# Performance work log

Hardware: AMD Instinct MI355X
Metric: run time of the kernel (lower is better)

The kernel has to match this reference:

```python
import jax, jax.numpy as jnp
import numpy as np

ALPHA = 0.2          # LeakyReLU negative slope
NEG_INF = -9e15      # mask value from the original code


def setup_inputs() -> dict:
    key = jax.random.key(0)
    k1, k2, k3, k4 = jax.random.split(key, 4)
    B, N, F_in, F_out = 8, 2048, 64, 64
    x = jax.random.normal(k1, (B, N, F_in), dtype=jnp.float32)
    adj = jax.random.randint(k2, (B, N, N), 0, 2, dtype=jnp.int32)
    W = jax.random.normal(k3, (F_in, F_out), dtype=jnp.float32)
    a = jax.random.normal(k4, (2 * F_out, 1), dtype=jnp.float32)
    return {"x": x, "adj": adj, "W": W, "a": a}


def reference(x, adj, W, a):
    # h: [B, N, F_out]
    h = jnp.matmul(x, W)
    F_out = W.shape[1]
    a1 = a[:F_out, 0]   # source half of attention vector
    a2 = a[F_out:, 0]   # target half
    # e_ij = leakyrelu(h_i . a1 + h_j . a2)  -- identical math to the
    # original cat([h_i, h_j]) @ a without materializing [B,N*N,2F].
    s1 = jnp.einsum('bnf,f->bn', h, a1)  # [B, N]
    s2 = jnp.einsum('bnf,f->bn', h, a2)  # [B, N]
    e = jax.nn.leaky_relu(s1[:, :, None] + s2[:, None, :], negative_slope=ALPHA)
    masked = jnp.where(adj > 0, e, NEG_INF)
    attention = jax.nn.softmax(masked, axis=2)  # [B, N, N]
    # dropout p=0.0 / eval mode -> identity
    h_prime = jnp.matmul(attention, h)          # [B, N, F_out]
    return jax.nn.elu(h_prime)                  # concat=True branch
```

## Files before the change

### kernel.cpp

```cpp
#include <hip/hip_runtime.h>
#include <cstdint>

#define LRELU_ALPHA 0.2f
#define NEG_INF -9000000000000000.0f
#define L2E 1.4426950408889634f

typedef __bf16 bf16x8 __attribute__((ext_vector_type(8)));
typedef unsigned short ushortx8 __attribute__((ext_vector_type(8)));
typedef float floatx4 __attribute__((ext_vector_type(4)));
typedef unsigned int uintx4 __attribute__((ext_vector_type(4)));

constexpr int Bb = 8, Nn = 2048, Ff = 64;
constexpr int TJ = 64;
constexpr int SEG = 8;
constexpr int SEGT = (Nn / TJ) / SEG;
constexpr int WIN = SEGT * TJ;
constexpr int WSTR = 264;
constexpr int NROWS = Bb * Nn;

__device__ __forceinline__ unsigned short f2bf(float f) {
    unsigned u = __builtin_bit_cast(unsigned, f);
    u = u + 0x7FFFu + ((u >> 16) & 1u);
    return (unsigned short)(u >> 16);
}

__device__ __forceinline__ unsigned cvt_pk_bf16(float lo, float hi) {
    unsigned r;
    asm("v_cvt_pk_bf16_f32 %0, %1, %2" : "=v"(r) : "v"(lo), "v"(hi));
    return r;
}

__global__ __launch_bounds__(256) void gat_prep(
    const float* __restrict__ x, const float* __restrict__ W, const float* __restrict__ a,
    unsigned short* __restrict__ hT, float* __restrict__ s1g, float* __restrict__ s2g)
{
    constexpr int STR2 = 36;
    __shared__ unsigned short hblk[64 * STR2];
    const int tid = threadIdx.x;
    const int blk = blockIdx.x;
    const int b  = blk >> 6;
    const int i0 = (blk & 63) * 32;
    const int w    = tid >> 6;
    const int lane = tid & 63;

    float wcol[64];
    #pragma unroll
    for (int k = 0; k < 64; ++k) wcol[k] = W[k * 64 + lane];
    const float a1 = a[lane], a2 = a[64 + lane];

    for (int r = 0; r < 8; ++r) {
        const int il = w * 8 + r;
        const int i  = i0 + il;
        const float* xrow = x + ((size_t)(b * Nn + i)) * 64;
        float h0 = 0.f, h1 = 0.f, h2 = 0.f, h3 = 0.f;
        #pragma unroll
        for (int k = 0; k < 64; k += 4) {
            h0 = fmaf(xrow[k],     wcol[k],     h0);
            h1 = fmaf(xrow[k + 1], wcol[k + 1], h1);
            h2 = fmaf(xrow[k + 2], wcol[k + 2], h2);
            h3 = fmaf(xrow[k + 3], wcol[k + 3], h3);
        }
        const float h = (h0 + h1) + (h2 + h3);
        float p1 = h * a1, p2 = h * a2;
        #pragma unroll
        for (int off = 32; off; off >>= 1) {
            p1 += __shfl_xor(p1, off);
            p2 += __shfl_xor(p2, off);
        }
        if (lane == 0) { s1g[b * Nn + i] = p1; s2g[b * Nn + i] = p2; }
        hblk[lane * STR2 + il] = f2bf(h);
    }
    __syncthreads();
    {
        const int f = tid >> 2, c = (tid & 3) * 8;
        uint4 v = *reinterpret_cast<const uint4*>(&hblk[f * STR2 + c]);
        *reinterpret_cast<uint4*>(hT + ((size_t)b * 64 + f) * Nn + i0 + c) = v;
    }
}

__global__ __launch_bounds__(256) void gat_attn(
    const int* __restrict__ adj, const unsigned short* __restrict__ hT,
    const float* __restrict__ s1g, const float* __restrict__ s2g,
    float* __restrict__ m_part, float* __restrict__ l_part, float* __restrict__ O_part)
{
    __shared__ unsigned short hT_lds[64 * WSTR];
    __shared__ float s2_lds[WIN];

    const int tid  = threadIdx.x;
    const int blk  = blockIdx.x;
    const int seg  = blk >> 8;
    const int grp  = blk & 255;
    const int gr0  = grp * 64;
    const int b    = gr0 >> 11;
    const int i0   = gr0 & 2047;
    const int w    = tid >> 6;
    const int lane = tid & 63;
    const int fl   = lane & 15;
    const int q    = lane >> 4;

    const int i = i0 + w * 16 + fl;
    const int j0w = seg * WIN;
    const unsigned short* hTb = hT + (size_t)b * 64 * Nn;

    uint4 stg[8];
    #pragma unroll
    for (int k = 0; k < 8; ++k) {
        const int c = tid + (k << 8);
        stg[k] = *reinterpret_cast<const uint4*>(
            hTb + (size_t)(c >> 5) * Nn + j0w + ((c & 31) << 3));
    }
    const float s2stg = s2g[b * Nn + j0w + tid];
    const float s1v = s1g[b * Nn + i];
    const int* adj_row = adj + ((size_t)(b * Nn + i)) * Nn;

    int4 adjv[4];
    {
        const int* arow = adj_row + j0w;
        const int4* ap0 = reinterpret_cast<const int4*>(arow + q * 8);
        adjv[0] = ap0[0]; adjv[1] = ap0[1];
        const int4* ap1 = reinterpret_cast<const int4*>(arow + 32 + q * 8);
        adjv[2] = ap1[0]; adjv[3] = ap1[1];
    }

    #pragma unroll
    for (int k = 0; k < 8; ++k) {
        const int c = tid + (k << 8);
        *reinterpret_cast<uint4*>(&hT_lds[(c >> 5) * WSTR + ((c & 31) << 3)]) = stg[k];
    }
    s2_lds[tid] = s2stg;
    __syncthreads();

    float m = NEG_INF, l = 0.f;
    floatx4 C[4] = {};

    for (int jt = 0; jt < SEGT; ++jt) {
        const int jloc = jt * TJ;

        int4 nadj[4] = {};
        if (jt + 1 < SEGT) {
            const int* nrow = adj_row + j0w + jloc + TJ;
            const int4* ap0 = reinterpret_cast<const int4*>(nrow + q * 8);
            nadj[0] = ap0[0]; nadj[1] = ap0[1];
            const int4* ap1 = reinterpret_cast<const int4*>(nrow + 32 + q * 8);
            nadj[2] = ap1[0]; nadj[3] = ap1[1];
        }

        float p[16];
        const int* av = reinterpret_cast<const int*>(adjv);
        #pragma unroll
        for (int t = 0; t < 2; ++t) {
            float s2v[8];
            *reinterpret_cast<float4*>(&s2v[0]) =
                *reinterpret_cast<const float4*>(&s2_lds[jloc + t * 32 + q * 8]);
            *reinterpret_cast<float4*>(&s2v[4]) =
                *reinterpret_cast<const float4*>(&s2_lds[jloc + t * 32 + q * 8 + 4]);
            #pragma unroll
            for (int jj = 0; jj < 8; ++jj) {
                float ev = s1v + s2v[jj];
                ev = fmaxf(ev, LRELU_ALPHA * ev);
                p[t * 8 + jj] = (av[t * 8 + jj] > 0) ? ev : NEG_INF;
            }
        }
        float tmax = p[0];
        #pragma unroll
        for (int k = 1; k < 16; ++k) tmax = fmaxf(tmax, p[k]);
        tmax = fmaxf(tmax, __shfl_xor(tmax, 16));
        tmax = fmaxf(tmax, __shfl_xor(tmax, 32));
        const float m_new = fmaxf(m, tmax);
        const float alpha_s = exp2f((m - m_new) * L2E);
        m = m_new;

        float tsum = 0.f;
        #pragma unroll
        for (int k = 0; k < 16; ++k) {
            p[k] = exp2f((p[k] - m_new) * L2E);
            tsum += p[k];
        }
        tsum += __shfl_xor(tsum, 16);
        tsum += __shfl_xor(tsum, 32);
        l = l * alpha_s + tsum;

        uintx4 pa, pb;
        #pragma unroll
        for (int d = 0; d < 4; ++d) {
            pa[d] = cvt_pk_bf16(p[2 * d],     p[2 * d + 1]);
            pb[d] = cvt_pk_bf16(p[8 + 2 * d], p[8 + 2 * d + 1]);
        }
        const bf16x8 A0 = __builtin_bit_cast(bf16x8, pa);
        const bf16x8 A1 = __builtin_bit_cast(bf16x8, pb);

        float ac[4];
        #pragma unroll
        for (int r = 0; r < 4; ++r) ac[r] = __shfl(alpha_s, q * 4 + r);
        #pragma unroll
        for (int u = 0; u < 4; ++u)
            #pragma unroll
            for (int r = 0; r < 4; ++r) C[u][r] *= ac[r];

        __builtin_amdgcn_s_setprio(1);
        #pragma unroll
        for (int u = 0; u < 4; ++u) {
            const bf16x8 B0 = *reinterpret_cast<const bf16x8*>(
                &hT_lds[(u * 16 + fl) * WSTR + jloc + q * 8]);
            C[u] = __builtin_amdgcn_mfma_f32_16x16x32_bf16(A0, B0, C[u], 0, 0, 0);
            const bf16x8 B1 = *reinterpret_cast<const bf16x8*>(
                &hT_lds[(u * 16 + fl) * WSTR + jloc + 32 + q * 8]);
            C[u] = __builtin_amdgcn_mfma_f32_16x16x32_bf16(A1, B1, C[u], 0, 0, 0);
        }
        __builtin_amdgcn_s_setprio(0);

        adjv[0] = nadj[0]; adjv[1] = nadj[1]; adjv[2] = nadj[2]; adjv[3] = nadj[3];
    }

    if (q == 0) {
        const int ri = b * Nn + i;
        m_part[seg * NROWS + ri] = m;
        l_part[seg * NROWS + ri] = l;
    }
    #pragma unroll
    for (int u = 0; u < 4; ++u) {
        #pragma unroll
        for (int r = 0; r < 4; ++r) {
            const int orow = i0 + w * 16 + q * 4 + r;
            O_part[((size_t)seg * NROWS + b * Nn + orow) * 64 + u * 16 + fl] = C[u][r];
        }
    }
}

__global__ __launch_bounds__(256) void gat_merge(
    const float* __restrict__ m_part, const float* __restrict__ l_part,
    const float* __restrict__ O_part, float* __restrict__ out)
{
    const int tid = threadIdx.x;
    const int ri  = blockIdx.x * 4 + (tid >> 6);
    const int f   = tid & 63;

    float mv[SEG];
    #pragma unroll
    for (int s = 0; s < SEG; ++s) mv[s] = m_part[s * NROWS + ri];
    float mstar = mv[0];
    #pragma unroll
    for (int s = 1; s < SEG; ++s) mstar = fmaxf(mstar, mv[s]);

    float lsum = 0.f, acc = 0.f;
    #pragma unroll
    for (int s = 0; s < SEG; ++s) {
        const float wgt = exp2f((mv[s] - mstar) * L2E);
        lsum += l_part[s * NROWS + ri] * wgt;
        acc  += O_part[((size_t)s * NROWS + ri) * 64 + f] * wgt;
    }
    float v = acc / lsum;
    v = (v > 0.f) ? v : (exp2f(v * L2E) - 1.f);
    out[(size_t)ri * 64 + f] = v;
}

extern "C" void kernel_launch(void* const* d_in, const int* in_sizes, int n_in,
                              void* d_out, int out_size, void* d_ws, size_t ws_size,
                              hipStream_t stream) {
    const float* x   = (const float*)d_in[0];
    const int*   adj = (const int*)d_in[1];
    const float* W   = (const float*)d_in[2];
    const float* a   = (const float*)d_in[3];
    float* out = (float*)d_out;

    char* p = (char*)d_ws;
    unsigned short* hT = (unsigned short*)p;  p += (size_t)Bb * 64 * Nn * sizeof(unsigned short);
    float* s1 = (float*)p;                    p += (size_t)NROWS * sizeof(float);
    float* s2 = (float*)p;                    p += (size_t)NROWS * sizeof(float);
    float* m_part = (float*)p;                p += (size_t)SEG * NROWS * sizeof(float);
    float* l_part = (float*)p;                p += (size_t)SEG * NROWS * sizeof(float);
    float* O_part = (float*)p;

    gat_prep<<<dim3(Bb * Nn / 32), dim3(256), 0, stream>>>(x, W, a, hT, s1, s2);
    gat_attn<<<dim3(SEG * (NROWS / 64)), dim3(256), 0, stream>>>(
        adj, hT, s1, s2, m_part, l_part, O_part);
    gat_merge<<<dim3(NROWS / 4), dim3(256), 0, stream>>>(m_part, l_part, O_part, out);
}
```

Measured before the change: 237.0 us.

## Cut j-split to two segments with double-staged hT windows and lazy rescale

Each block now covers 1024 columns in 2 segments instead of 8. It streams 256-column windows of hT and s2 through registers into LDS, prefetching the next window while computing the current one. This reduces the partial-result write and merge traffic and the grid size. The online-softmax rescale of the accumulators is skipped when no row max increases in the wave. In exchange there are fewer blocks (a 512 grid, down from 2048) and extra barriers per window.

```diff
diff --git a/kernel.cpp b/kernel.cpp
--- a/kernel.cpp
+++ b/kernel.cpp
@@ -6,15 +6,16 @@
 #define L2E 1.4426950408889634f
 
 typedef __bf16 bf16x8 __attribute__((ext_vector_type(8)));
-typedef unsigned short ushortx8 __attribute__((ext_vector_type(8)));
 typedef float floatx4 __attribute__((ext_vector_type(4)));
 typedef unsigned int uintx4 __attribute__((ext_vector_type(4)));
 
 constexpr int Bb = 8, Nn = 2048, Ff = 64;
 constexpr int TJ = 64;
-constexpr int SEG = 8;
-constexpr int SEGT = (Nn / TJ) / SEG;
-constexpr int WIN = SEGT * TJ;
+constexpr int SEG = 2;
+constexpr int SEGJ = Nn / SEG;
+constexpr int WIN = 256;
+constexpr int NW = SEGJ / WIN;
+constexpr int NTILE = SEGJ / TJ;
 constexpr int WSTR = 264;
 constexpr int NROWS = Bb * Nn;
 
@@ -99,117 +100,134 @@
     const int q    = lane >> 4;
 
     const int i = i0 + w * 16 + fl;
-    const int j0w = seg * WIN;
+    const int jseg0 = seg * SEGJ;
     const unsigned short* hTb = hT + (size_t)b * 64 * Nn;
+    const int* adj_row = adj + ((size_t)(b * Nn + i)) * Nn + jseg0;
+    const float* s2b = s2g + b * Nn + jseg0;
+    const float s1v = s1g[b * Nn + i];
 
     uint4 stg[8];
-    #pragma unroll
-    for (int k = 0; k < 8; ++k) {
-        const int c = tid + (k << 8);
-        stg[k] = *reinterpret_cast<const uint4*>(
-            hTb + (size_t)(c >> 5) * Nn + j0w + ((c & 31) << 3));
-    }
-    const float s2stg = s2g[b * Nn + j0w + tid];
-    const float s1v = s1g[b * Nn + i];
-    const int* adj_row = adj + ((size_t)(b * Nn + i)) * Nn;
-
-    int4 adjv[4];
-    {
-        const int* arow = adj_row + j0w;
+    float s2stg;
+
+    auto stage_issue = [&](int wn) {
+        const int jb = wn * WIN;
+        #pragma unroll
+        for (int k = 0; k < 8; ++k) {
+            const int c = tid + (k << 8);
+            stg[k] = *reinterpret_cast<const uint4*>(
+                hTb + (size_t)(c >> 5) * Nn + jseg0 + jb + ((c & 31) << 3));
+        }
+        s2stg = s2b[jb + tid];
+    };
+    auto stage_write = [&]() {
+        #pragma unroll
+        for (int k = 0; k < 8; ++k) {
+            const int c = tid + (k << 8);
+            *reinterpret_cast<uint4*>(&hT_lds[(c >> 5) * WSTR + ((c & 31) << 3)]) = stg[k];
+        }
+        s2_lds[tid] = s2stg;
+    };
+    auto adj_load = [&](int t, int4 (&av)[4]) {
+        const int* arow = adj_row + t * TJ;
         const int4* ap0 = reinterpret_cast<const int4*>(arow + q * 8);
-        adjv[0] = ap0[0]; adjv[1] = ap0[1];
+        av[0] = ap0[0]; av[1] = ap0[1];
         const int4* ap1 = reinterpret_cast<const int4*>(arow + 32 + q * 8);
-        adjv[2] = ap1[0]; adjv[3] = ap1[1];
-    }
-
-    #pragma unroll
-    for (int k = 0; k < 8; ++k) {
-        const int c = tid + (k << 8);
-        *reinterpret_cast<uint4*>(&hT_lds[(c >> 5) * WSTR + ((c & 31) << 3)]) = stg[k];
-    }
-    s2_lds[tid] = s2stg;
+        av[2] = ap1[0]; av[3] = ap1[1];
+    };
+
+    int4 adjv[4], nadj[4];
+    stage_issue(0);
+    adj_load(0, adjv);
+    stage_write();
     __syncthreads();
 
     float m = NEG_INF, l = 0.f;
     floatx4 C[4] = {};
 
-    for (int jt = 0; jt < SEGT; ++jt) {
-        const int jloc = jt * TJ;
-
-        int4 nadj[4] = {};
-        if (jt + 1 < SEGT) {
-            const int* nrow = adj_row + j0w + jloc + TJ;
-            const int4* ap0 = reinterpret_cast<const int4*>(nrow + q * 8);
-            nadj[0] = ap0[0]; nadj[1] = ap0[1];
-            const int4* ap1 = reinterpret_cast<const int4*>(nrow + 32 + q * 8);
-            nadj[2] = ap1[0]; nadj[3] = ap1[1];
-        }
-
-        float p[16];
-        const int* av = reinterpret_cast<const int*>(adjv);
-        #pragma unroll
-        for (int t = 0; t < 2; ++t) {
-            float s2v[8];
-            *reinterpret_cast<float4*>(&s2v[0]) =
-                *reinterpret_cast<const float4*>(&s2_lds[jloc + t * 32 + q * 8]);
-            *reinterpret_cast<float4*>(&s2v[4]) =
-                *reinterpret_cast<const float4*>(&s2_lds[jloc + t * 32 + q * 8 + 4]);
-            #pragma unroll
-            for (int jj = 0; jj < 8; ++jj) {
-                float ev = s1v + s2v[jj];
-                ev = fmaxf(ev, LRELU_ALPHA * ev);
-                p[t * 8 + jj] = (av[t * 8 + jj] > 0) ? ev : NEG_INF;
-            }
-        }
-        float tmax = p[0];
-        #pragma unroll
-        for (int k = 1; k < 16; ++k) tmax = fmaxf(tmax, p[k]);
-        tmax = fmaxf(tmax, __shfl_xor(tmax, 16));
-        tmax = fmaxf(tmax, __shfl_xor(tmax, 32));
-        const float m_new = fmaxf(m, tmax);
-        const float alpha_s = exp2f((m - m_new) * L2E);
-        m = m_new;
-
-        float tsum = 0.f;
-        #pragma unroll
-        for (int k = 0; k < 16; ++k) {
-            p[k] = exp2f((p[k] - m_new) * L2E);
-            tsum += p[k];
-        }
-        tsum += __shfl_xor(tsum, 16);
-        tsum += __shfl_xor(tsum, 32);
-        l = l * alpha_s + tsum;
-
-        uintx4 pa, pb;
-        #pragma unroll
-        for (int d = 0; d < 4; ++d) {
-            pa[d] = cvt_pk_bf16(p[2 * d],     p[2 * d + 1]);
-            pb[d] = cvt_pk_bf16(p[8 + 2 * d], p[8 + 2 * d + 1]);
-        }
-        const bf16x8 A0 = __builtin_bit_cast(bf16x8, pa);
-        const bf16x8 A1 = __builtin_bit_cast(bf16x8, pb);
-
-        float ac[4];
-        #pragma unroll
-        for (int r = 0; r < 4; ++r) ac[r] = __shfl(alpha_s, q * 4 + r);
-        #pragma unroll
-        for (int u = 0; u < 4; ++u)
-            #pragma unroll
-            for (int r = 0; r < 4; ++r) C[u][r] *= ac[r];
-
-        __builtin_amdgcn_s_setprio(1);
-        #pragma unroll
-        for (int u = 0; u < 4; ++u) {
-            const bf16x8 B0 = *reinterpret_cast<const bf16x8*>(
-                &hT_lds[(u * 16 + fl) * WSTR + jloc + q * 8]);
-            C[u] = __builtin_amdgcn_mfma_f32_16x16x32_bf16(A0, B0, C[u], 0, 0, 0);
-            const bf16x8 B1 = *reinterpret_cast<const bf16x8*>(
-                &hT_lds[(u * 16 + fl) * WSTR + jloc + 32 + q * 8]);
-            C[u] = __builtin_amdgcn_mfma_f32_16x16x32_bf16(A1, B1, C[u], 0, 0, 0);
-        }
-        __builtin_amdgcn_s_setprio(0);
-
-        adjv[0] = nadj[0]; adjv[1] = nadj[1]; adjv[2] = nadj[2]; adjv[3] = nadj[3];
+    for (int wn = 0; wn < NW; ++wn) {
+        if (wn + 1 < NW) stage_issue(wn + 1);
+
+        #pragma unroll
+        for (int jt = 0; jt < WIN / TJ; ++jt) {
+            const int t = wn * (WIN / TJ) + jt;
+            if (t + 1 < NTILE) adj_load(t + 1, nadj);
+            const int jloc = jt * TJ;
+
+            float p[16];
+            const int* av = reinterpret_cast<const int*>(adjv);
+            #pragma unroll
+            for (int tt = 0; tt < 2; ++tt) {
+                float s2v[8];
+                *reinterpret_cast<float4*>(&s2v[0]) =
+                    *reinterpret_cast<const float4*>(&s2_lds[jloc + tt * 32 + q * 8]);
+                *reinterpret_cast<float4*>(&s2v[4]) =
+                    *reinterpret_cast<const float4*>(&s2_lds[jloc + tt * 32 + q * 8 + 4]);
+                #pragma unroll
+                for (int jj = 0; jj < 8; ++jj) {
+                    float ev = s1v + s2v[jj];
+                    ev = fmaxf(ev, LRELU_ALPHA * ev);
+                    p[tt * 8 + jj] = (av[tt * 8 + jj] > 0) ? ev : NEG_INF;
+                }
+            }
+            float tmax = p[0];
+            #pragma unroll
+            for (int k = 1; k < 16; ++k) tmax = fmaxf(tmax, p[k]);
+            tmax = fmaxf(tmax, __shfl_xor(tmax, 16));
+            tmax = fmaxf(tmax, __shfl_xor(tmax, 32));
+            const float m_new = fmaxf(m, tmax);
+
+            if (__any(m_new > m)) {
+                const float alpha_s = exp2f((m - m_new) * L2E);
+                l *= alpha_s;
+                float ac[4];
+                #pragma unroll
+                for (int r = 0; r < 4; ++r) ac[r] = __shfl(alpha_s, q * 4 + r);
+                #pragma unroll
+                for (int u = 0; u < 4; ++u)
+                    #pragma unroll
+                    for (int r = 0; r < 4; ++r) C[u][r] *= ac[r];
+                m = m_new;
+            }
+
+            float tsum = 0.f;
+            #pragma unroll
+            for (int k = 0; k < 16; ++k) {
+                p[k] = exp2f((p[k] - m) * L2E);
+                tsum += p[k];
+            }
+            tsum += __shfl_xor(tsum, 16);
+            tsum += __shfl_xor(tsum, 32);
+            l += tsum;
+
+            uintx4 pa, pb;
+            #pragma unroll
+            for (int d = 0; d < 4; ++d) {
+                pa[d] = cvt_pk_bf16(p[2 * d],     p[2 * d + 1]);
+                pb[d] = cvt_pk_bf16(p[8 + 2 * d], p[8 + 2 * d + 1]);
+            }
+            const bf16x8 A0 = __builtin_bit_cast(bf16x8, pa);
+            const bf16x8 A1 = __builtin_bit_cast(bf16x8, pb);
+
+            __builtin_amdgcn_s_setprio(1);
+            #pragma unroll
+            for (int u = 0; u < 4; ++u) {
+                const bf16x8 B0 = *reinterpret_cast<const bf16x8*>(
+                    &hT_lds[(u * 16 + fl) * WSTR + jloc + q * 8]);
+                C[u] = __builtin_amdgcn_mfma_f32_16x16x32_bf16(A0, B0, C[u], 0, 0, 0);
+                const bf16x8 B1 = *reinterpret_cast<const bf16x8*>(
+                    &hT_lds[(u * 16 + fl) * WSTR + jloc + 32 + q * 8]);
+                C[u] = __builtin_amdgcn_mfma_f32_16x16x32_bf16(A1, B1, C[u], 0, 0, 0);
+            }
+            __builtin_amdgcn_s_setprio(0);
+
+            adjv[0] = nadj[0]; adjv[1] = nadj[1]; adjv[2] = nadj[2]; adjv[3] = nadj[3];
+        }
+
+        if (wn + 1 < NW) {
+            __syncthreads();
+            stage_write();
+            __syncthreads();
+        }
     }
 
     if (q == 0) {
```

Result: slower. 243.0 us (+2.5%).

## Fuse split-K merge into attention kernel with in-block segment reduction

Applied to the files above, without the earlier changes.

Restructures the attention kernel so each 512-thread block handles 16 rows, with 8 waves each covering one 256-column slice. The partial max, sum and output are merged in LDS inside the same block, which removes the separate merge kernel and the global m/l/O partial buffers. The hT and s2 tiles are now read straight from global memory/cache instead of being staged in LDS. Accumulator rescaling is skipped when no lane's running max grows. This trades LDS staging and the next-tile adjacency prefetch for less global traffic and one fewer launch, at the risk of more load latency in the inner loop.

```diff
diff --git a/kernel.cpp b/kernel.cpp
--- a/kernel.cpp
+++ b/kernel.cpp
@@ -6,16 +6,14 @@
 #define L2E 1.4426950408889634f
 
 typedef __bf16 bf16x8 __attribute__((ext_vector_type(8)));
-typedef unsigned short ushortx8 __attribute__((ext_vector_type(8)));
 typedef float floatx4 __attribute__((ext_vector_type(4)));
 typedef unsigned int uintx4 __attribute__((ext_vector_type(4)));
 
 constexpr int Bb = 8, Nn = 2048, Ff = 64;
 constexpr int TJ = 64;
-constexpr int SEG = 8;
-constexpr int SEGT = (Nn / TJ) / SEG;
-constexpr int WIN = SEGT * TJ;
-constexpr int WSTR = 264;
+constexpr int SEGW = 8;
+constexpr int SLICE = Nn / SEGW;
+constexpr int NT = SLICE / TJ;
 constexpr int NROWS = Bb * Nn;
 
 __device__ __forceinline__ unsigned short f2bf(float f) {
@@ -78,87 +76,59 @@
     }
 }
 
-__global__ __launch_bounds__(256) void gat_attn(
+__global__ __launch_bounds__(512, 6) void gat_attn(
     const int* __restrict__ adj, const unsigned short* __restrict__ hT,
     const float* __restrict__ s1g, const float* __restrict__ s2g,
-    float* __restrict__ m_part, float* __restrict__ l_part, float* __restrict__ O_part)
+    float* __restrict__ out)
 {
-    __shared__ unsigned short hT_lds[64 * WSTR];
-    __shared__ float s2_lds[WIN];
+    __shared__ float O_lds[SEGW][16][65];
+    __shared__ float m_lds[SEGW][16];
+    __shared__ float l_lds[SEGW][16];
 
     const int tid  = threadIdx.x;
     const int blk  = blockIdx.x;
-    const int seg  = blk >> 8;
-    const int grp  = blk & 255;
-    const int gr0  = grp * 64;
-    const int b    = gr0 >> 11;
-    const int i0   = gr0 & 2047;
-    const int w    = tid >> 6;
+    const int b    = blk >> 7;
+    const int i0   = (blk & 127) * 16;
+    const int s    = tid >> 6;
     const int lane = tid & 63;
     const int fl   = lane & 15;
     const int q    = lane >> 4;
 
-    const int i = i0 + w * 16 + fl;
-    const int j0w = seg * WIN;
-    const unsigned short* hTb = hT + (size_t)b * 64 * Nn;
-
-    uint4 stg[8];
-    #pragma unroll
-    for (int k = 0; k < 8; ++k) {
-        const int c = tid + (k << 8);
-        stg[k] = *reinterpret_cast<const uint4*>(
-            hTb + (size_t)(c >> 5) * Nn + j0w + ((c & 31) << 3));
-    }
-    const float s2stg = s2g[b * Nn + j0w + tid];
+    const int i = i0 + fl;
     const float s1v = s1g[b * Nn + i];
-    const int* adj_row = adj + ((size_t)(b * Nn + i)) * Nn;
-
-    int4 adjv[4];
-    {
-        const int* arow = adj_row + j0w;
-        const int4* ap0 = reinterpret_cast<const int4*>(arow + q * 8);
-        adjv[0] = ap0[0]; adjv[1] = ap0[1];
-        const int4* ap1 = reinterpret_cast<const int4*>(arow + 32 + q * 8);
-        adjv[2] = ap1[0]; adjv[3] = ap1[1];
-    }
-
-    #pragma unroll
-    for (int k = 0; k < 8; ++k) {
-        const int c = tid + (k << 8);
-        *reinterpret_cast<uint4*>(&hT_lds[(c >> 5) * WSTR + ((c & 31) << 3)]) = stg[k];
-    }
-    s2_lds[tid] = s2stg;
-    __syncthreads();
+    const int* adj_row = adj + ((size_t)(b * Nn + i)) * Nn + s * SLICE;
+    const unsigned short* hTb = hT + (size_t)b * 64 * Nn + s * SLICE;
+    const float* s2b = s2g + b * Nn + s * SLICE;
 
     float m = NEG_INF, l = 0.f;
     floatx4 C[4] = {};
 
-    for (int jt = 0; jt < SEGT; ++jt) {
+    for (int jt = 0; jt < NT; ++jt) {
         const int jloc = jt * TJ;
 
-        int4 nadj[4] = {};
-        if (jt + 1 < SEGT) {
-            const int* nrow = adj_row + j0w + jloc + TJ;
-            const int4* ap0 = reinterpret_cast<const int4*>(nrow + q * 8);
-            nadj[0] = ap0[0]; nadj[1] = ap0[1];
-            const int4* ap1 = reinterpret_cast<const int4*>(nrow + 32 + q * 8);
-            nadj[2] = ap1[0]; nadj[3] = ap1[1];
+        int4 adjv[4];
+        {
+            const int* arow = adj_row + jloc;
+            const int4* ap0 = reinterpret_cast<const int4*>(arow + q * 8);
+            adjv[0] = ap0[0]; adjv[1] = ap0[1];
+            const int4* ap1 = reinterpret_cast<const int4*>(arow + 32 + q * 8);
+            adjv[2] = ap1[0]; adjv[3] = ap1[1];
         }
 
         float p[16];
         const int* av = reinterpret_cast<const int*>(adjv);
         #pragma unroll
-        for (int t = 0; t < 2; ++t) {
+        for (int tt = 0; tt < 2; ++tt) {
             float s2v[8];
             *reinterpret_cast<float4*>(&s2v[0]) =
-                *reinterpret_cast<const float4*>(&s2_lds[jloc + t * 32 + q * 8]);
+                *reinterpret_cast<const float4*>(&s2b[jloc + tt * 32 + q * 8]);
             *reinterpret_cast<float4*>(&s2v[4]) =
-                *reinterpret_cast<const float4*>(&s2_lds[jloc + t * 32 + q * 8 + 4]);
+                *reinterpret_cast<const float4*>(&s2b[jloc + tt * 32 + q * 8 + 4]);
             #pragma unroll
             for (int jj = 0; jj < 8; ++jj) {
                 float ev = s1v + s2v[jj];
                 ev = fmaxf(ev, LRELU_ALPHA * ev);
-                p[t * 8 + jj] = (av[t * 8 + jj] > 0) ? ev : NEG_INF;
+                p[tt * 8 + jj] = (av[tt * 8 + jj] > 0) ? ev : NEG_INF;
             }
         }
         float tmax = p[0];
@@ -167,18 +137,29 @@
         tmax = fmaxf(tmax, __shfl_xor(tmax, 16));
         tmax = fmaxf(tmax, __shfl_xor(tmax, 32));
         const float m_new = fmaxf(m, tmax);
-        const float alpha_s = exp2f((m - m_new) * L2E);
-        m = m_new;
+
+        if (__any(m_new > m)) {
+            const float alpha_s = exp2f((m - m_new) * L2E);
+            l *= alpha_s;
+            float ac[4];
+            #pragma unroll
+            for (int r = 0; r < 4; ++r) ac[r] = __shfl(alpha_s, q * 4 + r);
+            #pragma unroll
+            for (int u = 0; u < 4; ++u)
+                #pragma unroll
+                for (int r = 0; r < 4; ++r) C[u][r] *= ac[r];
+            m = m_new;
+        }
 
         float tsum = 0.f;
         #pragma unroll
         for (int k = 0; k < 16; ++k) {
-            p[k] = exp2f((p[k] - m_new) * L2E);
+            p[k] = exp2f((p[k] - m) * L2E);
             tsum += p[k];
         }
         tsum += __shfl_xor(tsum, 16);
         tsum += __shfl_xor(tsum, 32);
-        l = l * alpha_s + tsum;
+        l += tsum;
 
         uintx4 pa, pb;
         #pragma unroll
@@ -189,69 +170,52 @@
         const bf16x8 A0 = __builtin_bit_cast(bf16x8, pa);
         const bf16x8 A1 = __builtin_bit_cast(bf16x8, pb);
 
-        float ac[4];
-        #pragma unroll
-        for (int r = 0; r < 4; ++r) ac[r] = __shfl(alpha_s, q * 4 + r);
-        #pragma unroll
-        for (int u = 0; u < 4; ++u)
-            #pragma unroll
-            for (int r = 0; r < 4; ++r) C[u][r] *= ac[r];
-
         __builtin_amdgcn_s_setprio(1);
         #pragma unroll
         for (int u = 0; u < 4; ++u) {
             const bf16x8 B0 = *reinterpret_cast<const bf16x8*>(
-                &hT_lds[(u * 16 + fl) * WSTR + jloc + q * 8]);
+                hTb + (size_t)(u * 16 + fl) * Nn + jloc + q * 8);
             C[u] = __builtin_amdgcn_mfma_f32_16x16x32_bf16(A0, B0, C[u], 0, 0, 0);
             const bf16x8 B1 = *reinterpret_cast<const bf16x8*>(
-                &hT_lds[(u * 16 + fl) * WSTR + jloc + 32 + q * 8]);
+                hTb + (size_t)(u * 16 + fl) * Nn + jloc + 32 + q * 8);
             C[u] = __builtin_amdgcn_mfma_f32_16x16x32_bf16(A1, B1, C[u], 0, 0, 0);
         }
         __builtin_amdgcn_s_setprio(0);
-
-        adjv[0] = nadj[0]; adjv[1] = nadj[1]; adjv[2] = nadj[2]; adjv[3] = nadj[3];
-    }
-
-    if (q == 0) {
-        const int ri = b * Nn + i;
-        m_part[seg * NROWS + ri] = m;
-        l_part[seg * NROWS + ri] = l;
-    }
-    #pragma unroll
-    for (int u = 0; u < 4; ++u) {
-        #pragma unroll
-        for (int r = 0; r < 4; ++r) {
-            const int orow = i0 + w * 16 + q * 4 + r;
-            O_part[((size_t)seg * NROWS + b * Nn + orow) * 64 + u * 16 + fl] = C[u][r];
-        }
-    }
-}
-
-__global__ __launch_bounds__(256) void gat_merge(
-    const float* __restrict__ m_part, const float* __restrict__ l_part,
-    const float* __restrict__ O_part, float* __restrict__ out)
-{
-    const int tid = threadIdx.x;
-    const int ri  = blockIdx.x * 4 + (tid >> 6);
-    const int f   = tid & 63;
-
-    float mv[SEG];
-    #pragma unroll
-    for (int s = 0; s < SEG; ++s) mv[s] = m_part[s * NROWS + ri];
+    }
+
+    #pragma unroll
+    for (int u = 0; u < 4; ++u)
+        #pragma unroll
+        for (int r = 0; r < 4; ++r)
+            O_lds[s][q * 4 + r][u * 16 + fl] = C[u][r];
+    if (q == 0) { m_lds[s][fl] = m; l_lds[s][fl] = l; }
+    __syncthreads();
+
+    const int row = tid >> 5;
+    const int f0  = (tid & 31) * 2;
+
+    float mv[SEGW];
+    #pragma unroll
+    for (int k = 0; k < SEGW; ++k) mv[k] = m_lds[k][row];
     float mstar = mv[0];
     #pragma unroll
-    for (int s = 1; s < SEG; ++s) mstar = fmaxf(mstar, mv[s]);
-
-    float lsum = 0.f, acc = 0.f;
-    #pragma unroll
-    for (int s = 0; s < SEG; ++s) {
-        const float wgt = exp2f((mv[s] - mstar) * L2E);
-        lsum += l_part[s * NROWS + ri] * wgt;
-        acc  += O_part[((size_t)s * NROWS + ri) * 64 + f] * wgt;
-    }
-    float v = acc / lsum;
-    v = (v > 0.f) ? v : (exp2f(v * L2E) - 1.f);
-    out[(size_t)ri * 64 + f] = v;
+    for (int k = 1; k < SEGW; ++k) mstar = fmaxf(mstar, mv[k]);
+
+    float lsum = 0.f, acc0 = 0.f, acc1 = 0.f;
+    #pragma unroll
+    for (int k = 0; k < SEGW; ++k) {
+        const float wgt = exp2f((mv[k] - mstar) * L2E);
+        lsum += l_lds[k][row] * wgt;
+        const float2 ov = *reinterpret_cast<const float2*>(&O_lds[k][row][f0]);
+        acc0 += ov.x * wgt;
+        acc1 += ov.y * wgt;
+    }
+    const float inv = 1.f / lsum;
+    float v0 = acc0 * inv, v1 = acc1 * inv;
+    v0 = (v0 > 0.f) ? v0 : (exp2f(v0 * L2E) - 1.f);
+    v1 = (v1 > 0.f) ? v1 : (exp2f(v1 * L2E) - 1.f);
+    float2 o2; o2.x = v0; o2.y = v1;
+    *reinterpret_cast<float2*>(&out[((size_t)(b * Nn + i0 + row)) * 64 + f0]) = o2;
 }
 
 extern "C" void kernel_launch(void* const* d_in, const int* in_sizes, int n_in,
@@ -266,13 +230,8 @@
     char* p = (char*)d_ws;
     unsigned short* hT = (unsigned short*)p;  p += (size_t)Bb * 64 * Nn * sizeof(unsigned short);
     float* s1 = (float*)p;                    p += (size_t)NROWS * sizeof(float);
-    float* s2 = (float*)p;                    p += (size_t)NROWS * sizeof(float);
-    float* m_part = (float*)p;                p += (size_t)SEG * NROWS * sizeof(float);
-    float* l_part = (float*)p;                p += (size_t)SEG * NROWS * sizeof(float);
-    float* O_part = (float*)p;
+    float* s2 = (float*)p;
 
     gat_prep<<<dim3(Bb * Nn / 32), dim3(256), 0, stream>>>(x, W, a, hT, s1, s2);
-    gat_attn<<<dim3(SEG * (NROWS / 64)), dim3(256), 0, stream>>>(
-        adj, hT, s1, s2, m_part, l_part, O_part);
-    gat_merge<<<dim3(NROWS / 4), dim3(256), 0, stream>>>(m_part, l_part, O_part, out);
-}
+    gat_attn<<<dim3(NROWS / 16), dim3(512), 0, stream>>>(adj, hT, s1, s2, out);
+}
```

Result: slower. 244.0 us (+3.0%).
